# Kernel tuning notes

Measured on AMD Instinct MI355X. Metric: run time of the kernel, lower is better.

Reference implementation:

```python
import jax, jax.numpy as jnp
import numpy as np

DIM = 1024
MEM = 512
HEAD = DIM // 2


def setup_inputs() -> dict:
    key = jax.random.key(0)
    k0, k1, k2, k3, k4 = jax.random.split(key, 5)
    x = jax.random.normal(k0, (4, 8192, DIM), dtype=jnp.float32)
    keys_real = jax.random.normal(k1, (MEM, HEAD), dtype=jnp.float32) * 0.02
    keys_imag = jax.random.normal(k2, (MEM, HEAD), dtype=jnp.float32) * 0.02
    values_real = jax.random.normal(k3, (MEM, HEAD), dtype=jnp.float32) * 0.02
    values_imag = jax.random.normal(k4, (MEM, HEAD), dtype=jnp.float32) * 0.02
    return {"x": x, "keys_real": keys_real, "keys_imag": keys_imag,
            "values_real": values_real, "values_imag": values_imag}


def reference(x, keys_real, keys_imag, values_real, values_imag):
    input_shape = x.shape
    temperature = HEAD ** (-0.5)
    x_flat = x.reshape(-1, DIM)                       # [N, dim]
    q, p = jnp.split(x_flat, 2, axis=-1)              # each [N, head]
    # dual real/imag score matmuls summed -> energy [N, mem]
    energy = jnp.einsum('nh,mh->nm', q, keys_real) + jnp.einsum('nh,mh->nm', p, keys_imag)
    attn = jax.nn.softmax(energy * temperature, axis=-1)
    out_real = jnp.einsum('nm,mh->nh', attn, values_real)
    out_imag = jnp.einsum('nm,mh->nh', attn, values_imag)
    return jnp.concatenate([out_real, out_imag], axis=-1).reshape(input_shape)
```

## Files before the change

### kernel.cpp

```cpp
#include <hip/hip_runtime.h>


#define DIMX   1024
#define MEMN   512
#define NROWS  32768
#define TEMP   0.04419417382415922f

typedef __bf16 bf16;
typedef __bf16 bf16x8 __attribute__((ext_vector_type(8)));
typedef float  f32x4  __attribute__((ext_vector_type(4)));

__device__ __forceinline__ void gload_lds16(const void* g, void* l) {
    __builtin_amdgcn_global_load_lds(
        (const __attribute__((address_space(1))) unsigned*)g,
        (__attribute__((address_space(3))) unsigned*)l,
        16, 0, 0);
}
__device__ __forceinline__ void gl_b16x8(bf16x8& d, const bf16* p) {
    asm volatile("global_load_dwordx4 %0, %1, off" : "=v"(d) : "v"(p));
}
__device__ __forceinline__ void gl_f32x4(f32x4& d, const float* p) {
    asm volatile("global_load_dwordx4 %0, %1, off" : "=v"(d) : "v"(p));
}
#define VMW(N)     do { asm volatile("s_waitcnt vmcnt(" #N ")" ::: "memory"); \
                        __builtin_amdgcn_sched_barrier(0); } while (0)
#define WAITBAR(N) do { asm volatile("s_waitcnt vmcnt(" #N ") lgkmcnt(0)\n\t" \
                        "s_barrier" ::: "memory");                            \
                        __builtin_amdgcn_sched_barrier(0); } while (0)
#define VMWBAR(N)  do { asm volatile("s_waitcnt vmcnt(" #N ")\n\t"            \
                        "s_barrier" ::: "memory");                            \
                        __builtin_amdgcn_sched_barrier(0); } while (0)

__global__ __launch_bounds__(256) void pack_kv_kernel(const float* __restrict__ kr,
                                                      const float* __restrict__ ki,
                                                      const float* __restrict__ vr,
                                                      const float* __restrict__ vi,
                                                      bf16* __restrict__ Kb,
                                                      bf16* __restrict__ Vb) {
    const int idx = blockIdx.x * 256 + threadIdx.x;
    const int e = idx & 7, l = (idx >> 3) & 63;
    const int lm = l & 15, g = l >> 4;
    {
        const int t = (idx >> 9) & 31, c = idx >> 14;
        const int row = t * 16 + lm, k = c * 32 + g * 8 + e;
        const float v = (k < 512) ? kr[row * 512 + k] : ki[row * 512 + (k - 512)];
        Kb[idx] = (bf16)v;
    }
    {
        const int t = (idx >> 9) & 63, c = idx >> 15;
        const int h = t * 16 + lm, m = c * 32 + g * 8 + e;
        const float v = (h < 512) ? vr[m * 512 + h] : vi[m * 512 + (h - 512)];
        Vb[idx] = (bf16)v;
    }
}

__global__ __launch_bounds__(256, 2) void energy_softmax_kernel(
        const float* __restrict__ x,
        const bf16*  __restrict__ Kb,
        bf16* __restrict__ attn) {
    __shared__ __align__(16) bf16 Xs[2][64 * 64];
    __shared__ float red[64][4][2];

    const int tid  = threadIdx.x;
    const int wv   = tid >> 6, lane = tid & 63;
    const int lm   = lane & 15, g = lane >> 4;
    const int rowB = blockIdx.x * 64;

    const int sr = tid >> 2, sc = tid & 3;
    const float* xsrc = x + (size_t)(rowB + sr) * DIMX + sc * 16;

    const bf16* kbase = Kb + (wv * 8) * 512 + lane * 8;

    f32x4 acc[4][8] = {};
    f32x4 xa0, xa1, xa2, xa3;
    bf16x8 kfA[8], kfB[8];

#define K_PREF(DST, C) { _Pragma("unroll") for (int j = 0; j < 8; ++j)         \
        gl_b16x8(DST[j], kbase + (size_t)(C) * 16384 + j * 512); }
#define X_PREF(P) { gl_f32x4(xa0, xsrc + (P) * 64);                            \
                    gl_f32x4(xa1, xsrc + (P) * 64 + 4);                        \
                    gl_f32x4(xa2, xsrc + (P) * 64 + 8);                        \
                    gl_f32x4(xa3, xsrc + (P) * 64 + 12); }
#define X_WR(B) { bf16x8 w0, w1;                                               \
    w0[0]=(bf16)xa0[0]; w0[1]=(bf16)xa0[1]; w0[2]=(bf16)xa0[2]; w0[3]=(bf16)xa0[3]; \
    w0[4]=(bf16)xa1[0]; w0[5]=(bf16)xa1[1]; w0[6]=(bf16)xa1[2]; w0[7]=(bf16)xa1[3]; \
    w1[0]=(bf16)xa2[0]; w1[1]=(bf16)xa2[1]; w1[2]=(bf16)xa2[2]; w1[3]=(bf16)xa2[3]; \
    w1[4]=(bf16)xa3[0]; w1[5]=(bf16)xa3[1]; w1[6]=(bf16)xa3[2]; w1[7]=(bf16)xa3[3]; \
    *(bf16x8*)((char*)Xs[B] + sr * 128 + (((2 * sc)     ^ (sr & 7)) << 4)) = w0; \
    *(bf16x8*)((char*)Xs[B] + sr * 128 + (((2 * sc + 1) ^ (sr & 7)) << 4)) = w1; }
#define COMPUTE_E(PB, S, KF) { bf16x8 af[4];                                   \
    _Pragma("unroll") for (int i = 0; i < 4; ++i) { const int r = i * 16 + lm; \
        af[i] = *(const bf16x8*)((const char*)Xs[PB] + r * 128                 \
                                 + (((((S) * 4) + g) ^ (r & 7)) << 4)); }      \
    __builtin_amdgcn_s_setprio(1);                                             \
    _Pragma("unroll") for (int i = 0; i < 4; ++i)                              \
        _Pragma("unroll") for (int j = 0; j < 8; ++j)                          \
            acc[i][j] = __builtin_amdgcn_mfma_f32_16x16x32_bf16(               \
                af[i], KF[j], acc[i][j], 0, 0, 0);                             \
    __builtin_amdgcn_s_setprio(0); }

    X_PREF(0);
    K_PREF(kfA, 0);
    VMW(8);
    X_WR(0);
    X_PREF(1);
    WAITBAR(12);

    for (int p = 0; p < 14; ++p) {
        const int pb = p & 1;
        K_PREF(kfB, 2 * p + 1);
        VMW(12);
        COMPUTE_E(pb, 0, kfA);
        K_PREF(kfA, 2 * p + 2);
        VMW(8);
        COMPUTE_E(pb, 1, kfB);
        X_WR(pb ^ 1);
        X_PREF(p + 2);
        WAITBAR(12);
    }
    K_PREF(kfB, 29);
    VMW(12);
    COMPUTE_E(0, 0, kfA);
    K_PREF(kfA, 30);
    VMW(8);
    COMPUTE_E(0, 1, kfB);
    X_WR(1);
    WAITBAR(8);
    K_PREF(kfB, 31);
    VMW(8);
    COMPUTE_E(1, 0, kfA);
    VMW(0);
    COMPUTE_E(1, 1, kfB);

#undef K_PREF
#undef X_PREF
#undef X_WR
#undef COMPUTE_E

    float fac[4][4];
    #pragma unroll
    for (int i = 0; i < 4; ++i) {
        #pragma unroll
        for (int rg = 0; rg < 4; ++rg) {
            float m = acc[i][0][rg] * TEMP;
            #pragma unroll
            for (int j = 1; j < 8; ++j) m = fmaxf(m, acc[i][j][rg] * TEMP);
            m = fmaxf(m, __shfl_xor(m, 1));
            m = fmaxf(m, __shfl_xor(m, 2));
            m = fmaxf(m, __shfl_xor(m, 4));
            m = fmaxf(m, __shfl_xor(m, 8));
            float s = 0.f;
            #pragma unroll
            for (int j = 0; j < 8; ++j) {
                const float v = __expf(acc[i][j][rg] * TEMP - m);
                acc[i][j][rg] = v;
                s += v;
            }
            s += __shfl_xor(s, 1);
            s += __shfl_xor(s, 2);
            s += __shfl_xor(s, 4);
            s += __shfl_xor(s, 8);
            const int rr = i * 16 + g * 4 + rg;
            if (lm == 0) { red[rr][wv][0] = m; red[rr][wv][1] = s; }
            fac[i][rg] = m;
        }
    }
    __syncthreads();
    #pragma unroll
    for (int i = 0; i < 4; ++i) {
        #pragma unroll
        for (int rg = 0; rg < 4; ++rg) {
            const int rr = i * 16 + g * 4 + rg;
            const float m0 = red[rr][0][0], s0 = red[rr][0][1];
            const float m1 = red[rr][1][0], s1 = red[rr][1][1];
            const float m2 = red[rr][2][0], s2 = red[rr][2][1];
            const float m3 = red[rr][3][0], s3 = red[rr][3][1];
            const float M  = fmaxf(fmaxf(m0, m1), fmaxf(m2, m3));
            const float S  = s0 * __expf(m0 - M) + s1 * __expf(m1 - M)
                           + s2 * __expf(m2 - M) + s3 * __expf(m3 - M);
            fac[i][rg] = __expf(fac[i][rg] - M) / S;
        }
    }
    #pragma unroll
    for (int i = 0; i < 4; ++i) {
        #pragma unroll
        for (int rg = 0; rg < 4; ++rg) {
            const size_t rr = (size_t)(rowB + i * 16 + g * 4 + rg);
            bf16* p = attn + rr * MEMN + wv * 128 + lm;
            const float f = fac[i][rg];
            #pragma unroll
            for (int j = 0; j < 8; ++j)
                p[j * 16] = (bf16)(acc[i][j][rg] * f);
        }
    }
}

__global__ __launch_bounds__(256, 2) void gemm2_kernel(const bf16* __restrict__ A,
                                                       const bf16* __restrict__ Vb,
                                                       float* __restrict__ C) {
    __shared__ __align__(16) bf16 As[8][128 * 32];

    const int cpx = gridDim.x >> 3;
    const int l   = ((int)blockIdx.x & 7) * cpx + ((int)blockIdx.x >> 3);
    const int bx  = l & 7, by = l >> 3;

    const int tid  = threadIdx.x;
    const int wave = tid >> 6, lane = tid & 63;
    const int lm   = lane & 15, g = lane >> 4;
    const int rowB = by * 128;
    const int wrow = (wave >> 1) * 64;

    const bf16* vbase = Vb + (bx * 8 + (wave & 1) * 4) * 512 + lane * 8;

    f32x4 acc[4][4] = {};
    bf16x8 bfA[4], bfB[4], bfC[4], bfD[4];

#define A_STAGE(BI, C0) { _Pragma("unroll") for (int li = 0; li < 2; ++li) {    \
        const int q = wave * 2 + li;                                            \
        const int r = q * 16 + (lane >> 2);                                     \
        const int ch = lane & 3;                                                \
        gload_lds16(A + (size_t)(rowB + r) * 512 + (C0) * 32                    \
                      + ((ch ^ ((r >> 1) & 3)) << 3),                           \
                    (char*)As[BI] + q * 1024); } }
#define B_PREF(DST, C0) { _Pragma("unroll") for (int j = 0; j < 4; ++j)         \
        gl_b16x8(DST[j], vbase + (size_t)(C0) * 32768 + j * 512); }
#define COMPUTE_G(BI, BF) { bf16x8 af[4];                                       \
    _Pragma("unroll") for (int i = 0; i < 4; ++i) {                             \
        const int r = wrow + i * 16 + lm;                                       \
        af[i] = *(const bf16x8*)((const char*)As[BI] + r * 64                   \
                                 + ((g ^ ((r >> 1) & 3)) << 4)); }              \
    __builtin_amdgcn_s_setprio(1);                                              \
    _Pragma("unroll") for (int i = 0; i < 4; ++i)                               \
        _Pragma("unroll") for (int j = 0; j < 4; ++j)                           \
            acc[i][j] = __builtin_amdgcn_mfma_f32_16x16x32_bf16(                \
                af[i], BF[j], acc[i][j], 0, 0, 0);                              \
    __builtin_amdgcn_s_setprio(0); }
#define PERIOD_G(P, C0F, C1F, N0F, N1F)                                         \
    B_PREF(N0F, 2 * (P) + 2);                                                   \
    B_PREF(N1F, 2 * (P) + 3);                                        \
    VMW(12);                                         \
    COMPUTE_G((2 * (P)) & 7, C0F);                                              \
    COMPUTE_G((2 * (P) + 1) & 7, C1F);                                          \
    A_STAGE((2 * (P) + 4) & 7, 2 * (P) + 4);                                    \
    A_STAGE((2 * (P) + 5) & 7, 2 * (P) + 5);                         \
    VMWBAR(12);

    A_STAGE(0, 0);  A_STAGE(1, 1);
    B_PREF(bfA, 0); B_PREF(bfB, 1);
    A_STAGE(2, 2);  A_STAGE(3, 3);
    VMWBAR(12);

    for (int p = 0; p < 6; p += 2) {
        PERIOD_G(p,     bfA, bfB, bfC, bfD);
        PERIOD_G(p + 1, bfC, bfD, bfA, bfB);
    }
    B_PREF(bfC, 14);
    B_PREF(bfD, 15);
    VMW(12);
    COMPUTE_G(4, bfA);
    COMPUTE_G(5, bfB);
    VMWBAR(8);
    VMW(0);
    COMPUTE_G(6, bfC);
    COMPUTE_G(7, bfD);

#undef A_STAGE
#undef B_PREF
#undef COMPUTE_G
#undef PERIOD_G

    const int r0 = rowB + wrow + g * 4;
    const int c0 = bx * 128 + (wave & 1) * 64 + lm;
    #pragma unroll
    for (int i = 0; i < 4; ++i) {
        #pragma unroll
        for (int j = 0; j < 4; ++j) {
            #pragma unroll
            for (int r = 0; r < 4; ++r)
                C[(size_t)(r0 + i * 16 + r) * DIMX + (c0 + j * 16)] = acc[i][j][r];
        }
    }
}

extern "C" void kernel_launch(void* const* d_in, const int* in_sizes, int n_in,
                              void* d_out, int out_size, void* d_ws, size_t ws_size,
                              hipStream_t stream) {
    const float* x  = (const float*)d_in[0];
    const float* kr = (const float*)d_in[1];
    const float* ki = (const float*)d_in[2];
    const float* vr = (const float*)d_in[3];
    const float* vi = (const float*)d_in[4];
    float* out = (float*)d_out;

    char* ws = (char*)d_ws;
    bf16* Kb   = (bf16*)ws;
    bf16* Vb   = (bf16*)(ws + 1048576);
    bf16* attn = (bf16*)(ws + 2097152);

    pack_kv_kernel<<<2048, 256, 0, stream>>>(kr, ki, vr, vi, Kb, Vb);
    energy_softmax_kernel<<<512, 256, 0, stream>>>(x, Kb, attn);
    gemm2_kernel<<<2048, 256, 0, stream>>>(attn, Vb, out);
}
```

Baseline: 289.4 us.

## Fuse softmax output and PV matmul into one kernel via LDS-resident attention tile

Merges the energy/softmax kernel with the second GEMM. Each 64-row block writes its normalized bf16 attention tile into swizzled LDS and then multiplies it against the packed V matrix directly, so the intermediate attention buffer never goes to global memory and one launch is removed. The cost is that each block now streams all of V (1024 columns) from global/L2 with only 512 blocks, with less parallelism and a 64KB shared allocation that may lower occupancy.

After: 274.0 us. 5.3% less time.

```diff
diff --git a/kernel.cpp b/kernel.cpp
--- a/kernel.cpp
+++ b/kernel.cpp
@@ -10,12 +10,6 @@
 typedef __bf16 bf16x8 __attribute__((ext_vector_type(8)));
 typedef float  f32x4  __attribute__((ext_vector_type(4)));
 
-__device__ __forceinline__ void gload_lds16(const void* g, void* l) {
-    __builtin_amdgcn_global_load_lds(
-        (const __attribute__((address_space(1))) unsigned*)g,
-        (__attribute__((address_space(3))) unsigned*)l,
-        16, 0, 0);
-}
 __device__ __forceinline__ void gl_b16x8(bf16x8& d, const bf16* p) {
     asm volatile("global_load_dwordx4 %0, %1, off" : "=v"(d) : "v"(p));
 }
@@ -25,9 +19,6 @@
 #define VMW(N)     do { asm volatile("s_waitcnt vmcnt(" #N ")" ::: "memory"); \
                         __builtin_amdgcn_sched_barrier(0); } while (0)
 #define WAITBAR(N) do { asm volatile("s_waitcnt vmcnt(" #N ") lgkmcnt(0)\n\t" \
-                        "s_barrier" ::: "memory");                            \
-                        __builtin_amdgcn_sched_barrier(0); } while (0)
-#define VMWBAR(N)  do { asm volatile("s_waitcnt vmcnt(" #N ")\n\t"            \
                         "s_barrier" ::: "memory");                            \
                         __builtin_amdgcn_sched_barrier(0); } while (0)
 
@@ -54,12 +45,14 @@
     }
 }
 
-__global__ __launch_bounds__(256, 2) void energy_softmax_kernel(
+__global__ __launch_bounds__(256, 2) void fused_kernel(
         const float* __restrict__ x,
         const bf16*  __restrict__ Kb,
-        bf16* __restrict__ attn) {
-    __shared__ __align__(16) bf16 Xs[2][64 * 64];
-    __shared__ float red[64][4][2];
+        const bf16*  __restrict__ Vb,
+        float* __restrict__ out) {
+    __shared__ __align__(16) char smem[65536];
+    float (*red)[4][2] = (float (*)[4][2])(smem + 16384);
+    char* Pl = smem;
 
     const int tid  = threadIdx.x;
     const int wv   = tid >> 6, lane = tid & 63;
@@ -86,11 +79,11 @@
     w0[4]=(bf16)xa1[0]; w0[5]=(bf16)xa1[1]; w0[6]=(bf16)xa1[2]; w0[7]=(bf16)xa1[3]; \
     w1[0]=(bf16)xa2[0]; w1[1]=(bf16)xa2[1]; w1[2]=(bf16)xa2[2]; w1[3]=(bf16)xa2[3]; \
     w1[4]=(bf16)xa3[0]; w1[5]=(bf16)xa3[1]; w1[6]=(bf16)xa3[2]; w1[7]=(bf16)xa3[3]; \
-    *(bf16x8*)((char*)Xs[B] + sr * 128 + (((2 * sc)     ^ (sr & 7)) << 4)) = w0; \
-    *(bf16x8*)((char*)Xs[B] + sr * 128 + (((2 * sc + 1) ^ (sr & 7)) << 4)) = w1; }
+    *(bf16x8*)(smem + (B) * 8192 + sr * 128 + (((2 * sc)     ^ (sr & 7)) << 4)) = w0; \
+    *(bf16x8*)(smem + (B) * 8192 + sr * 128 + (((2 * sc + 1) ^ (sr & 7)) << 4)) = w1; }
 #define COMPUTE_E(PB, S, KF) { bf16x8 af[4];                                   \
     _Pragma("unroll") for (int i = 0; i < 4; ++i) { const int r = i * 16 + lm; \
-        af[i] = *(const bf16x8*)((const char*)Xs[PB] + r * 128                 \
+        af[i] = *(const bf16x8*)(smem + (PB) * 8192 + r * 128                  \
                                  + (((((S) * 4) + g) ^ (r & 7)) << 4)); }      \
     __builtin_amdgcn_s_setprio(1);                                             \
     _Pragma("unroll") for (int i = 0; i < 4; ++i)                              \
@@ -181,105 +174,74 @@
             fac[i][rg] = __expf(fac[i][rg] - M) / S;
         }
     }
+    __syncthreads();
+
+    {
+        const int cb = wv * 16 + (lm >> 3);
+        const int ce = (lm & 7) * 2;
+        #pragma unroll
+        for (int i = 0; i < 4; ++i) {
+            #pragma unroll
+            for (int rg = 0; rg < 4; ++rg) {
+                const int row = i * 16 + g * 4 + rg;
+                const int rx  = row & 7;
+                const float f = fac[i][rg];
+                char* prow = Pl + row * 1024 + ce;
+                #pragma unroll
+                for (int j = 0; j < 8; ++j)
+                    *(bf16*)(prow + (((cb + j * 2) ^ rx) << 4))
+                        = (bf16)(acc[i][j][rg] * f);
+            }
+        }
+    }
+    __syncthreads();
+
+#define PV_COMPUTE(BF, KS) { bf16x8 af[4];                                     \
+    _Pragma("unroll") for (int i = 0; i < 4; ++i) { const int r = i * 16 + lm; \
+        af[i] = *(const bf16x8*)(Pl + r * 1024                                 \
+                                 + ((((KS) * 4 + g) ^ (r & 7)) << 4)); }       \
+    __builtin_amdgcn_s_setprio(1);                                             \
+    _Pragma("unroll") for (int i = 0; i < 4; ++i)                              \
+        _Pragma("unroll") for (int j = 0; j < 8; ++j)                          \
+            acc[i][j] = __builtin_amdgcn_mfma_f32_16x16x32_bf16(               \
+                af[i], BF[j], acc[i][j], 0, 0, 0);                             \
+    __builtin_amdgcn_s_setprio(0); }
+#define V_PREF(DST, KS) { _Pragma("unroll") for (int j = 0; j < 8; ++j)        \
+        gl_b16x8(DST[j], vb + (size_t)(KS) * 32768 + j * 512); }
+
     #pragma unroll
-    for (int i = 0; i < 4; ++i) {
-        #pragma unroll
-        for (int rg = 0; rg < 4; ++rg) {
-            const size_t rr = (size_t)(rowB + i * 16 + g * 4 + rg);
-            bf16* p = attn + rr * MEMN + wv * 128 + lm;
-            const float f = fac[i][rg];
+    for (int h = 0; h < 2; ++h) {
+        #pragma unroll
+        for (int i = 0; i < 4; ++i)
             #pragma unroll
             for (int j = 0; j < 8; ++j)
-                p[j * 16] = (bf16)(acc[i][j][rg] * f);
-        }
-    }
-}
-
-__global__ __launch_bounds__(256, 2) void gemm2_kernel(const bf16* __restrict__ A,
-                                                       const bf16* __restrict__ Vb,
-                                                       float* __restrict__ C) {
-    __shared__ __align__(16) bf16 As[8][128 * 32];
-
-    const int cpx = gridDim.x >> 3;
-    const int l   = ((int)blockIdx.x & 7) * cpx + ((int)blockIdx.x >> 3);
-    const int bx  = l & 7, by = l >> 3;
-
-    const int tid  = threadIdx.x;
-    const int wave = tid >> 6, lane = tid & 63;
-    const int lm   = lane & 15, g = lane >> 4;
-    const int rowB = by * 128;
-    const int wrow = (wave >> 1) * 64;
-
-    const bf16* vbase = Vb + (bx * 8 + (wave & 1) * 4) * 512 + lane * 8;
-
-    f32x4 acc[4][4] = {};
-    bf16x8 bfA[4], bfB[4], bfC[4], bfD[4];
-
-#define A_STAGE(BI, C0) { _Pragma("unroll") for (int li = 0; li < 2; ++li) {    \
-        const int q = wave * 2 + li;                                            \
-        const int r = q * 16 + (lane >> 2);                                     \
-        const int ch = lane & 3;                                                \
-        gload_lds16(A + (size_t)(rowB + r) * 512 + (C0) * 32                    \
-                      + ((ch ^ ((r >> 1) & 3)) << 3),                           \
-                    (char*)As[BI] + q * 1024); } }
-#define B_PREF(DST, C0) { _Pragma("unroll") for (int j = 0; j < 4; ++j)         \
-        gl_b16x8(DST[j], vbase + (size_t)(C0) * 32768 + j * 512); }
-#define COMPUTE_G(BI, BF) { bf16x8 af[4];                                       \
-    _Pragma("unroll") for (int i = 0; i < 4; ++i) {                             \
-        const int r = wrow + i * 16 + lm;                                       \
-        af[i] = *(const bf16x8*)((const char*)As[BI] + r * 64                   \
-                                 + ((g ^ ((r >> 1) & 3)) << 4)); }              \
-    __builtin_amdgcn_s_setprio(1);                                              \
-    _Pragma("unroll") for (int i = 0; i < 4; ++i)                               \
-        _Pragma("unroll") for (int j = 0; j < 4; ++j)                           \
-            acc[i][j] = __builtin_amdgcn_mfma_f32_16x16x32_bf16(                \
-                af[i], BF[j], acc[i][j], 0, 0, 0);                              \
-    __builtin_amdgcn_s_setprio(0); }
-#define PERIOD_G(P, C0F, C1F, N0F, N1F)                                         \
-    B_PREF(N0F, 2 * (P) + 2);                                                   \
-    B_PREF(N1F, 2 * (P) + 3);                                        \
-    VMW(12);                                         \
-    COMPUTE_G((2 * (P)) & 7, C0F);                                              \
-    COMPUTE_G((2 * (P) + 1) & 7, C1F);                                          \
-    A_STAGE((2 * (P) + 4) & 7, 2 * (P) + 4);                                    \
-    A_STAGE((2 * (P) + 5) & 7, 2 * (P) + 5);                         \
-    VMWBAR(12);
-
-    A_STAGE(0, 0);  A_STAGE(1, 1);
-    B_PREF(bfA, 0); B_PREF(bfB, 1);
-    A_STAGE(2, 2);  A_STAGE(3, 3);
-    VMWBAR(12);
-
-    for (int p = 0; p < 6; p += 2) {
-        PERIOD_G(p,     bfA, bfB, bfC, bfD);
-        PERIOD_G(p + 1, bfC, bfD, bfA, bfB);
-    }
-    B_PREF(bfC, 14);
-    B_PREF(bfD, 15);
-    VMW(12);
-    COMPUTE_G(4, bfA);
-    COMPUTE_G(5, bfB);
-    VMWBAR(8);
-    VMW(0);
-    COMPUTE_G(6, bfC);
-    COMPUTE_G(7, bfD);
-
-#undef A_STAGE
-#undef B_PREF
-#undef COMPUTE_G
-#undef PERIOD_G
-
-    const int r0 = rowB + wrow + g * 4;
-    const int c0 = bx * 128 + (wave & 1) * 64 + lm;
-    #pragma unroll
-    for (int i = 0; i < 4; ++i) {
-        #pragma unroll
-        for (int j = 0; j < 4; ++j) {
-            #pragma unroll
-            for (int r = 0; r < 4; ++r)
-                C[(size_t)(r0 + i * 16 + r) * DIMX + (c0 + j * 16)] = acc[i][j][r];
-        }
-    }
+                acc[i][j] = (f32x4){0.f, 0.f, 0.f, 0.f};
+
+        const bf16* vb = Vb + (size_t)(wv * 16 + h * 8) * 512 + lane * 8;
+        bf16x8 bv0[8], bv1[8];
+        V_PREF(bv0, 0);
+        for (int ks = 0; ks < 14; ks += 2) {
+            V_PREF(bv1, ks + 1); VMW(8); PV_COMPUTE(bv0, ks);
+            V_PREF(bv0, ks + 2); VMW(8); PV_COMPUTE(bv1, ks + 1);
+        }
+        V_PREF(bv1, 15); VMW(8); PV_COMPUTE(bv0, 14);
+        VMW(0);          PV_COMPUTE(bv1, 15);
+
+        const int c0 = wv * 256 + h * 128 + lm;
+        #pragma unroll
+        for (int i = 0; i < 4; ++i) {
+            #pragma unroll
+            for (int j = 0; j < 8; ++j) {
+                #pragma unroll
+                for (int rg = 0; rg < 4; ++rg)
+                    out[(size_t)(rowB + i * 16 + g * 4 + rg) * DIMX
+                        + (c0 + j * 16)] = acc[i][j][rg];
+            }
+        }
+    }
+
+#undef PV_COMPUTE
+#undef V_PREF
 }
 
 extern "C" void kernel_launch(void* const* d_in, const int* in_sizes, int n_in,
@@ -293,11 +255,9 @@
     float* out = (float*)d_out;
 
     char* ws = (char*)d_ws;
-    bf16* Kb   = (bf16*)ws;
-    bf16* Vb   = (bf16*)(ws + 1048576);
-    bf16* attn = (bf16*)(ws + 2097152);
+    bf16* Kb = (bf16*)ws;
+    bf16* Vb = (bf16*)(ws + 1048576);
 
     pack_kv_kernel<<<2048, 256, 0, stream>>>(kr, ki, vr, vi, Kb, Vb);
-    energy_softmax_kernel<<<512, 256, 0, stream>>>(x, Kb, attn);
-    gemm2_kernel<<<2048, 256, 0, stream>>>(attn, Vb, out);
-}
+    fused_kernel<<<512, 256, 0, stream>>>(x, Kb, Vb, out);
+}
```
